# Optimization experiments

Measured on AMD Instinct MI355X. Metric: run time of the kernel, lower is better.

Reference implementation:

```python
import jax, jax.numpy as jnp
import numpy as np

N_IN = 100000   # active input voxels
N_OUT = 200000  # active output voxels after stride-2 transposed conv
K = 27          # 3x3x3 kernel offsets
INC = 64
OUTC = 64
EPS = 1e-5


def setup_inputs() -> dict:
    key = jax.random.key(0)
    ks = jax.random.split(key, 6)
    return dict(
        feats=jax.random.normal(ks[0], (N_IN, INC), jnp.float32),
        weight=jax.random.normal(ks[1], (K, INC, OUTC), jnp.float32) * 0.05,
        # kernel map: per offset, which input voxel writes to which output voxel
        in_idx=jax.random.randint(ks[2], (K, N_IN), 0, N_IN, jnp.int32),
        out_idx=jax.random.randint(ks[3], (K, N_IN), 0, N_OUT, jnp.int32),
        gamma=jnp.ones((OUTC,), jnp.float32),
        beta=jnp.zeros((OUTC,), jnp.float32),
        running_mean=jax.random.normal(ks[4], (OUTC,), jnp.float32) * 0.1,
        running_var=jax.random.uniform(ks[5], (OUTC,), jnp.float32, minval=0.5, maxval=1.5),
    )


def reference(feats, weight, in_idx, out_idx, gamma, beta, running_mean, running_var):
    """Sparse transposed conv3d (gather-matmul-scatter over kernel offsets)
    followed by eval-mode BatchNorm and ReLU, matching
    torchsparse Conv3d(transposed=True) -> BatchNorm -> ReLU(inplace)."""

    def step(out, per_offset):
        w_k, ii, oi = per_offset                 # [INC,OUTC], [M], [M]
        part = feats[ii] @ w_k                   # gather + GEMM: [M, OUTC]
        return out.at[oi].add(part), None        # scatter-add into outputs

    out0 = jnp.zeros((N_OUT, OUTC), feats.dtype)
    out, _ = jax.lax.scan(step, out0, (weight, in_idx, out_idx))

    inv_std = jax.lax.rsqrt(running_var + EPS)
    y = (out - running_mean) * (inv_std * gamma) + beta
    return jax.nn.relu(y)
```

## Files before the change

kernel.cpp:

```cpp
#include <hip/hip_runtime.h>
#include <hip/hip_bf16.h>
#include <stdint.h>

#define NIN    100000
#define NOUT   200000
#define KOFF   27
#define C      64
#define NPAIR  (KOFF * NIN)
#define EPS    1e-5f
#define NCRS   391
#define CAPC   7680
#define NBIN   128
#define IPB_F  2048
#define ACCW   65
#define FIXS   262144.0f
#define FIXI   (1.0f / 262144.0f)

typedef __attribute__((ext_vector_type(8))) short bf16x8;
typedef __attribute__((ext_vector_type(4))) float f32x4;

__global__ __launch_bounds__(256)
void cvt_bf16_kernel(const float* __restrict__ src, ushort* __restrict__ dst, int n8)
{
    int t = blockIdx.x * 256 + threadIdx.x;
    if (t >= n8) return;
    const float4* s4 = reinterpret_cast<const float4*>(src) + (size_t)t * 2;
    float4 a = s4[0], b = s4[1];
    float v[8] = {a.x, a.y, a.z, a.w, b.x, b.y, b.z, b.w};
    union { ushort u[8]; uint4 q; } pk;
    #pragma unroll
    for (int j = 0; j < 8; ++j) {
        __hip_bfloat16 h = __float2bfloat16(v[j]);
        pk.u[j] = *reinterpret_cast<ushort*>(&h);
    }
    reinterpret_cast<uint4*>(dst)[t] = pk.q;
}

__global__ __launch_bounds__(256)
void cvt_wfrag_kernel(const float* __restrict__ w, ushort* __restrict__ wfrag)
{
    int t = blockIdx.x * 256 + threadIdx.x;
    if (t >= KOFF * 4 * 2 * 64) return;
    const int lane = t & 63;
    const int f    = t >> 6;
    const int kc   = f & 1;
    const int nt   = (f >> 1) & 3;
    const int k    = f >> 3;
    const int m16  = lane & 15;
    const int q    = lane >> 4;
    union { ushort u[8]; uint4 v; } pk;
    #pragma unroll
    for (int j = 0; j < 8; ++j) {
        const int ci = kc * 32 + 8 * q + j;
        const int co = nt * 16 + m16;
        __hip_bfloat16 h = __float2bfloat16(w[(size_t)k * 4096 + ci * 64 + co]);
        pk.u[j] = *reinterpret_cast<ushort*>(&h);
    }
    reinterpret_cast<uint4*>(wfrag)[t] = pk.v;
}

__global__ __launch_bounds__(256)
void bin_coarse_kernel(const int* __restrict__ in_idx, const int* __restrict__ out_idx,
                       int* __restrict__ gcur, uint32_t* __restrict__ binned)
{
    __shared__ uint32_t staged[IPB_F];
    __shared__ ushort   sbkt[IPB_F];
    __shared__ int hist[NCRS];
    __shared__ int lbase[NCRS];
    __shared__ int gd[NCRS];
    __shared__ int cur[NCRS];
    __shared__ int s[256];

    const int t  = threadIdx.x;
    const int t0 = blockIdx.x * IPB_F;
    int n = NPAIR - t0;
    if (n < 0) n = 0;
    if (n > IPB_F) n = IPB_F;

    for (int i = t; i < NCRS; i += 256) hist[i] = 0;
    __syncthreads();

    #pragma unroll 4
    for (int j = 0; j < IPB_F / 256; ++j) {
        int i = j * 256 + t;
        if (i < n) atomicAdd(&hist[out_idx[t0 + i] >> 9], 1);
    }
    __syncthreads();

    {
        const int i0 = 2 * t, i1 = 2 * t + 1;
        int v0 = (i0 < NCRS) ? hist[i0] : 0;
        int v1 = (i1 < NCRS) ? hist[i1] : 0;
        s[t] = v0 + v1;
        __syncthreads();
        for (int off = 1; off < 256; off <<= 1) {
            int x = (t >= off) ? s[t - off] : 0;
            __syncthreads();
            s[t] += x;
            __syncthreads();
        }
        int tb = s[t] - (v0 + v1);
        if (i0 < NCRS) lbase[i0] = tb;
        if (i1 < NCRS) lbase[i1] = tb + v0;
    }
    __syncthreads();

    for (int i = t; i < NCRS; i += 256) {
        int cnt = hist[i];
        int gb  = cnt ? atomicAdd(&gcur[i], cnt) : 0;
        gd[i]   = gb - lbase[i];
        cur[i]  = lbase[i];
    }
    __syncthreads();

    #pragma unroll 4
    for (int j = 0; j < IPB_F / 256; ++j) {
        int i = j * 256 + t;
        if (i < n) {
            int tt  = t0 + i;
            int oi  = out_idx[tt];
            int k   = tt / NIN;
            int bkt = oi >> 9;
            int pos = atomicAdd(&cur[bkt], 1);
            staged[pos] = ((uint32_t)(oi & 511) << 22)
                        | ((uint32_t)k << 17)
                        | (uint32_t)in_idx[tt];
            sbkt[pos] = (ushort)bkt;
        }
    }
    __syncthreads();

    for (int i = t; i < n; i += 256) {
        int b  = sbkt[i];
        int gp = gd[b] + i;
        if ((unsigned)gp < (unsigned)CAPC)
            binned[(size_t)b * CAPC + gp] = staged[i];
    }
}

__global__ __launch_bounds__(256)
void bin_fine_kernel(const int* __restrict__ gcur, uint32_t* __restrict__ binned,
                     int* __restrict__ foff)
{
    __shared__ uint32_t staged[CAPC];
    __shared__ int hist[NBIN], base[NBIN + 1], cur[NBIN];

    const int cb = blockIdx.x;
    const int t  = threadIdx.x;
    uint32_t* seg = binned + (size_t)cb * CAPC;
    int n = gcur[cb];
    if (n > CAPC) n = CAPC;

    if (t < NBIN) hist[t] = 0;
    __syncthreads();
    for (int i = t; i < n; i += 256) {
        uint32_t pl = seg[i];
        int b = (int)(((pl >> 29) & 3) * 32 + ((pl >> 17) & 31));
        atomicAdd(&hist[b], 1);
    }
    __syncthreads();
    if (t < NBIN) base[t + 1] = hist[t];
    __syncthreads();
    for (int off = 1; off < NBIN; off <<= 1) {
        int x = 0;
        if (t < NBIN && t >= off) x = base[t + 1 - off];
        __syncthreads();
        if (t < NBIN) base[t + 1] += x;
        __syncthreads();
    }
    if (t == 0) base[0] = 0;
    __syncthreads();
    if (t < NBIN) cur[t] = base[t + 1] - hist[t];
    __syncthreads();
    for (int i = t; i < n; i += 256) {
        uint32_t pl = seg[i];
        int b = (int)(((pl >> 29) & 3) * 32 + ((pl >> 17) & 31));
        int pos = atomicAdd(&cur[b], 1);
        staged[pos] = pl;
    }
    __syncthreads();
    for (int i = t; i < n; i += 256) seg[i] = staged[i];
    if (t <= NBIN) foff[(size_t)cb * (NBIN + 1) + t] = base[t];
}

__global__ __launch_bounds__(256)
void fused_conv_kernel(const ushort* __restrict__ featsb,
                       const ushort* __restrict__ wfragb,
                       const uint32_t* __restrict__ binned,
                       const int* __restrict__ foff,
                       const float* __restrict__ gamma,
                       const float* __restrict__ beta,
                       const float* __restrict__ mean,
                       const float* __restrict__ var,
                       float* __restrict__ out)
{
    __shared__ int acc[128 * ACCW];

    const int cb   = blockIdx.x;
    const int fb   = blockIdx.y;
    const int t    = threadIdx.x;
    const int wave = t >> 6;
    const int lane = t & 63;
    const int m16  = lane & 15;
    const int q    = lane >> 4;

    for (int i = t; i < 128 * ACCW; i += 256) acc[i] = 0;
    __syncthreads();

    const uint32_t* seg = binned + (size_t)cb * CAPC;
    const int* fo = foff + (size_t)cb * (NBIN + 1) + fb * 32;
    const bf16x8* wf = reinterpret_cast<const bf16x8*>(wfragb);

    for (int k = wave; k < KOFF; k += 4) {
        const int js = fo[k], je = fo[k + 1];
        if (js >= je) continue;

        bf16x8 xf[4][2];
        #pragma unroll
        for (int nt = 0; nt < 4; ++nt)
            #pragma unroll
            for (int kc = 0; kc < 2; ++kc)
                xf[nt][kc] = wf[(size_t)((k * 4 + nt) * 2 + kc) * 64 + lane];

        for (int base = js; base < je; base += 32) {
            const int idxA    = base + m16;
            const bool validA = idxA < je;
            const uint32_t plA = seg[validA ? idxA : je - 1];
            const int iiA = plA & 0x1FFFF;
            const int lrA = (int)((plA >> 22) & 127);
            const ushort* frA = featsb + (size_t)iiA * C;
            bf16x8 yA0 = *reinterpret_cast<const bf16x8*>(frA + 8 * q);
            bf16x8 yA1 = *reinterpret_cast<const bf16x8*>(frA + 32 + 8 * q);
            if (!validA) { yA0 = bf16x8{0,0,0,0,0,0,0,0}; yA1 = bf16x8{0,0,0,0,0,0,0,0}; }

            const bool doB = (base + 16) < je;
            bf16x8 yB0, yB1;
            int lrB = 0;
            if (doB) {
                const int idxB    = base + 16 + m16;
                const bool validB = idxB < je;
                const uint32_t plB = seg[validB ? idxB : je - 1];
                const int iiB = plB & 0x1FFFF;
                lrB = (int)((plB >> 22) & 127);
                const ushort* frB = featsb + (size_t)iiB * C;
                yB0 = *reinterpret_cast<const bf16x8*>(frB + 8 * q);
                yB1 = *reinterpret_cast<const bf16x8*>(frB + 32 + 8 * q);
                if (!validB) { yB0 = bf16x8{0,0,0,0,0,0,0,0}; yB1 = bf16x8{0,0,0,0,0,0,0,0}; }
            }

            f32x4 a0 = {0,0,0,0}, a1 = {0,0,0,0}, a2 = {0,0,0,0}, a3 = {0,0,0,0};
            a0 = __builtin_amdgcn_mfma_f32_16x16x32_bf16(xf[0][0], yA0, a0, 0, 0, 0);
            a1 = __builtin_amdgcn_mfma_f32_16x16x32_bf16(xf[1][0], yA0, a1, 0, 0, 0);
            a2 = __builtin_amdgcn_mfma_f32_16x16x32_bf16(xf[2][0], yA0, a2, 0, 0, 0);
            a3 = __builtin_amdgcn_mfma_f32_16x16x32_bf16(xf[3][0], yA0, a3, 0, 0, 0);
            a0 = __builtin_amdgcn_mfma_f32_16x16x32_bf16(xf[0][1], yA1, a0, 0, 0, 0);
            a1 = __builtin_amdgcn_mfma_f32_16x16x32_bf16(xf[1][1], yA1, a1, 0, 0, 0);
            a2 = __builtin_amdgcn_mfma_f32_16x16x32_bf16(xf[2][1], yA1, a2, 0, 0, 0);
            a3 = __builtin_amdgcn_mfma_f32_16x16x32_bf16(xf[3][1], yA1, a3, 0, 0, 0);

            int* arowA = acc + lrA * ACCW + q * 4;
            #pragma unroll
            for (int r = 0; r < 4; ++r)
                atomicAdd(&arowA[ 0 + r], __float2int_rn(a0[r] * FIXS));
            #pragma unroll
            for (int r = 0; r < 4; ++r)
                atomicAdd(&arowA[16 + r], __float2int_rn(a1[r] * FIXS));
            #pragma unroll
            for (int r = 0; r < 4; ++r)
                atomicAdd(&arowA[32 + r], __float2int_rn(a2[r] * FIXS));
            #pragma unroll
            for (int r = 0; r < 4; ++r)
                atomicAdd(&arowA[48 + r], __float2int_rn(a3[r] * FIXS));

            if (doB) {
                f32x4 b0 = {0,0,0,0}, b1 = {0,0,0,0}, b2 = {0,0,0,0}, b3 = {0,0,0,0};
                b0 = __builtin_amdgcn_mfma_f32_16x16x32_bf16(xf[0][0], yB0, b0, 0, 0, 0);
                b1 = __builtin_amdgcn_mfma_f32_16x16x32_bf16(xf[1][0], yB0, b1, 0, 0, 0);
                b2 = __builtin_amdgcn_mfma_f32_16x16x32_bf16(xf[2][0], yB0, b2, 0, 0, 0);
                b3 = __builtin_amdgcn_mfma_f32_16x16x32_bf16(xf[3][0], yB0, b3, 0, 0, 0);
                b0 = __builtin_amdgcn_mfma_f32_16x16x32_bf16(xf[0][1], yB1, b0, 0, 0, 0);
                b1 = __builtin_amdgcn_mfma_f32_16x16x32_bf16(xf[1][1], yB1, b1, 0, 0, 0);
                b2 = __builtin_amdgcn_mfma_f32_16x16x32_bf16(xf[2][1], yB1, b2, 0, 0, 0);
                b3 = __builtin_amdgcn_mfma_f32_16x16x32_bf16(xf[3][1], yB1, b3, 0, 0, 0);

                int* arowB = acc + lrB * ACCW + q * 4;
                #pragma unroll
                for (int r = 0; r < 4; ++r)
                    atomicAdd(&arowB[ 0 + r], __float2int_rn(b0[r] * FIXS));
                #pragma unroll
                for (int r = 0; r < 4; ++r)
                    atomicAdd(&arowB[16 + r], __float2int_rn(b1[r] * FIXS));
                #pragma unroll
                for (int r = 0; r < 4; ++r)
                    atomicAdd(&arowB[32 + r], __float2int_rn(b2[r] * FIXS));
                #pragma unroll
                for (int r = 0; r < 4; ++r)
                    atomicAdd(&arowB[48 + r], __float2int_rn(b3[r] * FIXS));
            }
        }
    }
    __syncthreads();

    const int cp = t & 15;
    float sc[4], sh[4];
    #pragma unroll
    for (int r = 0; r < 4; ++r) {
        const int c = cp * 4 + r;
        float s = gamma[c] * rsqrtf(var[c] + EPS);
        sc[r] = s;
        sh[r] = beta[c] - mean[c] * s;
    }
    float4* out4 = reinterpret_cast<float4*>(out);
    #pragma unroll
    for (int rep = 0; rep < 8; ++rep) {
        const int i   = t + rep * 256;
        const int rl  = i >> 4;
        const int row = cb * 512 + fb * 128 + rl;
        if (row < NOUT) {
            const int* ap = &acc[rl * ACCW + cp * 4];
            float v0 = fmaf((float)ap[0] * FIXI, sc[0], sh[0]); v0 = v0 > 0.f ? v0 : 0.f;
            float v1 = fmaf((float)ap[1] * FIXI, sc[1], sh[1]); v1 = v1 > 0.f ? v1 : 0.f;
            float v2 = fmaf((float)ap[2] * FIXI, sc[2], sh[2]); v2 = v2 > 0.f ? v2 : 0.f;
            float v3 = fmaf((float)ap[3] * FIXI, sc[3], sh[3]); v3 = v3 > 0.f ? v3 : 0.f;
            out4[(size_t)row * 16 + cp] = make_float4(v0, v1, v2, v3);
        }
    }
}

__global__ __launch_bounds__(256)
void conv_scatter_kernel(const float* __restrict__ feats,
                         const float* __restrict__ weight,
                         const int*   __restrict__ in_idx,
                         const int*   __restrict__ out_idx,
                         float*       __restrict__ out)
{
    const int k    = blockIdx.y;
    const int lane = threadIdx.x & 63;
    const int wave = threadIdx.x >> 6;
    const int wavesInGrid = gridDim.x * 4;
    const int waveId      = blockIdx.x * 4 + wave;

    const float* wk = weight + (size_t)k * C * C + lane;
    float w[C];
    #pragma unroll
    for (int ci = 0; ci < C; ++ci) w[ci] = wk[(size_t)ci * C];

    const int* ii_k = in_idx  + (size_t)k * NIN;
    const int* oi_k = out_idx + (size_t)k * NIN;

    for (int r = waveId; r < NIN; r += wavesInGrid) {
        const int ii = ii_k[r];
        const int oi = oi_k[r];
        const float4* frow = reinterpret_cast<const float4*>(feats + (size_t)ii * C);
        float acc = 0.0f;
        #pragma unroll
        for (int j = 0; j < C / 4; ++j) {
            float4 f = frow[j];
            acc = fmaf(f.x, w[4 * j + 0], acc);
            acc = fmaf(f.y, w[4 * j + 1], acc);
            acc = fmaf(f.z, w[4 * j + 2], acc);
            acc = fmaf(f.w, w[4 * j + 3], acc);
        }
        atomicAdd(out + (size_t)oi * C + lane, acc);
    }
}

__global__ __launch_bounds__(256)
void bn_relu_kernel(float* __restrict__ out,
                    const float* __restrict__ gamma,
                    const float* __restrict__ beta,
                    const float* __restrict__ mean,
                    const float* __restrict__ var)
{
    const int total4 = NOUT * C / 4;
    int idx = blockIdx.x * blockDim.x + threadIdx.x;
    if (idx >= total4) return;
    const int c0 = (idx * 4) & (C - 1);
    float sc[4], sh[4];
    #pragma unroll
    for (int j = 0; j < 4; ++j) {
        const int c  = c0 + j;
        const float s = gamma[c] * rsqrtf(var[c] + EPS);
        sc[j] = s;
        sh[j] = beta[c] - mean[c] * s;
    }
    float4* p = reinterpret_cast<float4*>(out) + idx;
    float4 v = *p;
    v.x = fmaf(v.x, sc[0], sh[0]); v.x = v.x > 0.f ? v.x : 0.f;
    v.y = fmaf(v.y, sc[1], sh[1]); v.y = v.y > 0.f ? v.y : 0.f;
    v.z = fmaf(v.z, sc[2], sh[2]); v.z = v.z > 0.f ? v.z : 0.f;
    v.w = fmaf(v.w, sc[3], sh[3]); v.w = v.w > 0.f ? v.w : 0.f;
    *p = v;
}

extern "C" void kernel_launch(void* const* d_in, const int* in_sizes, int n_in,
                              void* d_out, int out_size, void* d_ws, size_t ws_size,
                              hipStream_t stream) {
    const float* feats   = (const float*)d_in[0];
    const float* weight  = (const float*)d_in[1];
    const int*   in_idx  = (const int*)  d_in[2];
    const int*   out_idx = (const int*)  d_in[3];
    const float* gamma   = (const float*)d_in[4];
    const float* beta    = (const float*)d_in[5];
    const float* rmean   = (const float*)d_in[6];
    const float* rvar    = (const float*)d_in[7];
    float* out = (float*)d_out;

    auto align = [](size_t x) { return (x + 255) & ~(size_t)255; };

    size_t a = 0;
    size_t oBin = a; a += align((size_t)NCRS * CAPC * 4);
    size_t oGc  = a; a += align((size_t)NCRS * 4);
    size_t oFo  = a; a += align((size_t)NCRS * (NBIN + 1) * 4);
    size_t oFb  = a; a += align((size_t)NIN * C * 2);
    size_t oWf  = a; a += align((size_t)KOFF * 4 * 2 * 64 * 16);

    if (ws_size < a) {
        hipMemsetAsync(out, 0, (size_t)out_size * sizeof(float), stream);
        dim3 grid(512, KOFF);
        conv_scatter_kernel<<<grid, 256, 0, stream>>>(feats, weight, in_idx, out_idx, out);
        const int total4 = NOUT * C / 4;
        bn_relu_kernel<<<(total4 + 255) / 256, 256, 0, stream>>>(out, gamma, beta, rmean, rvar);
        return;
    }

    char* ws = (char*)d_ws;
    uint32_t* binned = (uint32_t*)(ws + oBin);
    int* gcur        = (int*)(ws + oGc);
    int* foff        = (int*)(ws + oFo);
    ushort* featsb   = (ushort*)(ws + oFb);
    ushort* wfragb   = (ushort*)(ws + oWf);

    {
        int n8f = NIN * C / 8;
        cvt_bf16_kernel<<<(n8f + 255) / 256, 256, 0, stream>>>(feats, featsb, n8f);
        int nwf = KOFF * 4 * 2 * 64;
        cvt_wfrag_kernel<<<(nwf + 255) / 256, 256, 0, stream>>>(weight, wfragb);
    }

    hipMemsetAsync(gcur, 0, (size_t)NCRS * sizeof(int), stream);
    {
        int nbC = (NPAIR + IPB_F - 1) / IPB_F;
        bin_coarse_kernel<<<nbC, 256, 0, stream>>>(in_idx, out_idx, gcur, binned);
        bin_fine_kernel<<<NCRS, 256, 0, stream>>>(gcur, binned, foff);
    }

    {
        dim3 grid(NCRS, 4);
        fused_conv_kernel<<<grid, 256, 0, stream>>>(featsb, wfragb, binned, foff,
                                                    gamma, beta, rmean, rvar, out);
    }
}
```

Baseline: 187.9 us.

## Split output channels across a third grid dimension and fold fixed-point scale into inputs

Adds blockIdx.z to split the 64 output channels into two halves, so each block keeps a half-width LDS accumulator (33 ints per row) and holds only the weight fragments for its half. This doubles the block count and halves the LDS footprint per block to raise occupancy and reduce atomic contention per block. The fixed-point scale is moved into the bf16 conversion by multiplying both feats and weights by 512, which removes the per-element multiply before the integer atomics. The cost is that every feature-row gather is repeated in both channel halves, and the BN scale and shift are now recomputed per output element.

Measured after the change: 201.9 us. +7.5%, slower.

```diff
diff --git a/kernel.cpp b/kernel.cpp
--- a/kernel.cpp
+++ b/kernel.cpp
@@ -12,8 +12,7 @@
 #define CAPC   7680
 #define NBIN   128
 #define IPB_F  2048
-#define ACCW   65
-#define FIXS   262144.0f
+#define ACW    33
 #define FIXI   (1.0f / 262144.0f)
 
 typedef __attribute__((ext_vector_type(8))) short bf16x8;
@@ -30,7 +29,7 @@
     union { ushort u[8]; uint4 q; } pk;
     #pragma unroll
     for (int j = 0; j < 8; ++j) {
-        __hip_bfloat16 h = __float2bfloat16(v[j]);
+        __hip_bfloat16 h = __float2bfloat16(v[j] * 512.0f);
         pk.u[j] = *reinterpret_cast<ushort*>(&h);
     }
     reinterpret_cast<uint4*>(dst)[t] = pk.q;
@@ -53,7 +52,7 @@
     for (int j = 0; j < 8; ++j) {
         const int ci = kc * 32 + 8 * q + j;
         const int co = nt * 16 + m16;
-        __hip_bfloat16 h = __float2bfloat16(w[(size_t)k * 4096 + ci * 64 + co]);
+        __hip_bfloat16 h = __float2bfloat16(w[(size_t)k * 4096 + ci * 64 + co] * 512.0f);
         pk.u[j] = *reinterpret_cast<ushort*>(&h);
     }
     reinterpret_cast<uint4*>(wfrag)[t] = pk.v;
@@ -194,17 +193,18 @@
                        const float* __restrict__ var,
                        float* __restrict__ out)
 {
-    __shared__ int acc[128 * ACCW];
+    __shared__ int acc[128 * ACW];
 
     const int cb   = blockIdx.x;
     const int fb   = blockIdx.y;
+    const int zc   = blockIdx.z;
     const int t    = threadIdx.x;
     const int wave = t >> 6;
     const int lane = t & 63;
     const int m16  = lane & 15;
     const int q    = lane >> 4;
 
-    for (int i = t; i < 128 * ACCW; i += 256) acc[i] = 0;
+    for (int i = t; i < 128 * ACW; i += 256) acc[i] = 0;
     __syncthreads();
 
     const uint32_t* seg = binned + (size_t)cb * CAPC;
@@ -215,12 +215,12 @@
         const int js = fo[k], je = fo[k + 1];
         if (js >= je) continue;
 
-        bf16x8 xf[4][2];
+        bf16x8 xf[2][2];
         #pragma unroll
-        for (int nt = 0; nt < 4; ++nt)
+        for (int ntl = 0; ntl < 2; ++ntl)
             #pragma unroll
             for (int kc = 0; kc < 2; ++kc)
-                xf[nt][kc] = wf[(size_t)((k * 4 + nt) * 2 + kc) * 64 + lane];
+                xf[ntl][kc] = wf[(size_t)((k * 4 + zc * 2 + ntl) * 2 + kc) * 64 + lane];
 
         for (int base = js; base < je; base += 32) {
             const int idxA    = base + m16;
@@ -234,7 +234,7 @@
             if (!validA) { yA0 = bf16x8{0,0,0,0,0,0,0,0}; yA1 = bf16x8{0,0,0,0,0,0,0,0}; }
 
             const bool doB = (base + 16) < je;
-            bf16x8 yB0, yB1;
+            bf16x8 yB0 = {0,0,0,0,0,0,0,0}, yB1 = {0,0,0,0,0,0,0,0};
             int lrB = 0;
             if (doB) {
                 const int idxB    = base + 16 + m16;
@@ -248,81 +248,60 @@
                 if (!validB) { yB0 = bf16x8{0,0,0,0,0,0,0,0}; yB1 = bf16x8{0,0,0,0,0,0,0,0}; }
             }
 
-            f32x4 a0 = {0,0,0,0}, a1 = {0,0,0,0}, a2 = {0,0,0,0}, a3 = {0,0,0,0};
-            a0 = __builtin_amdgcn_mfma_f32_16x16x32_bf16(xf[0][0], yA0, a0, 0, 0, 0);
-            a1 = __builtin_amdgcn_mfma_f32_16x16x32_bf16(xf[1][0], yA0, a1, 0, 0, 0);
-            a2 = __builtin_amdgcn_mfma_f32_16x16x32_bf16(xf[2][0], yA0, a2, 0, 0, 0);
-            a3 = __builtin_amdgcn_mfma_f32_16x16x32_bf16(xf[3][0], yA0, a3, 0, 0, 0);
-            a0 = __builtin_amdgcn_mfma_f32_16x16x32_bf16(xf[0][1], yA1, a0, 0, 0, 0);
-            a1 = __builtin_amdgcn_mfma_f32_16x16x32_bf16(xf[1][1], yA1, a1, 0, 0, 0);
-            a2 = __builtin_amdgcn_mfma_f32_16x16x32_bf16(xf[2][1], yA1, a2, 0, 0, 0);
-            a3 = __builtin_amdgcn_mfma_f32_16x16x32_bf16(xf[3][1], yA1, a3, 0, 0, 0);
-
-            int* arowA = acc + lrA * ACCW + q * 4;
-            #pragma unroll
-            for (int r = 0; r < 4; ++r)
-                atomicAdd(&arowA[ 0 + r], __float2int_rn(a0[r] * FIXS));
-            #pragma unroll
-            for (int r = 0; r < 4; ++r)
-                atomicAdd(&arowA[16 + r], __float2int_rn(a1[r] * FIXS));
-            #pragma unroll
-            for (int r = 0; r < 4; ++r)
-                atomicAdd(&arowA[32 + r], __float2int_rn(a2[r] * FIXS));
-            #pragma unroll
-            for (int r = 0; r < 4; ++r)
-                atomicAdd(&arowA[48 + r], __float2int_rn(a3[r] * FIXS));
-
-            if (doB) {
-                f32x4 b0 = {0,0,0,0}, b1 = {0,0,0,0}, b2 = {0,0,0,0}, b3 = {0,0,0,0};
-                b0 = __builtin_amdgcn_mfma_f32_16x16x32_bf16(xf[0][0], yB0, b0, 0, 0, 0);
-                b1 = __builtin_amdgcn_mfma_f32_16x16x32_bf16(xf[1][0], yB0, b1, 0, 0, 0);
-                b2 = __builtin_amdgcn_mfma_f32_16x16x32_bf16(xf[2][0], yB0, b2, 0, 0, 0);
-                b3 = __builtin_amdgcn_mfma_f32_16x16x32_bf16(xf[3][0], yB0, b3, 0, 0, 0);
-                b0 = __builtin_amdgcn_mfma_f32_16x16x32_bf16(xf[0][1], yB1, b0, 0, 0, 0);
-                b1 = __builtin_amdgcn_mfma_f32_16x16x32_bf16(xf[1][1], yB1, b1, 0, 0, 0);
-                b2 = __builtin_amdgcn_mfma_f32_16x16x32_bf16(xf[2][1], yB1, b2, 0, 0, 0);
-                b3 = __builtin_amdgcn_mfma_f32_16x16x32_bf16(xf[3][1], yB1, b3, 0, 0, 0);
-
-                int* arowB = acc + lrB * ACCW + q * 4;
+            {
+                f32x4 c0 = {0,0,0,0}, c1 = {0,0,0,0};
+                c0 = __builtin_amdgcn_mfma_f32_16x16x32_bf16(xf[0][0], yA0, c0, 0, 0, 0);
+                c1 = __builtin_amdgcn_mfma_f32_16x16x32_bf16(xf[1][0], yA0, c1, 0, 0, 0);
+                c0 = __builtin_amdgcn_mfma_f32_16x16x32_bf16(xf[0][1], yA1, c0, 0, 0, 0);
+                c1 = __builtin_amdgcn_mfma_f32_16x16x32_bf16(xf[1][1], yA1, c1, 0, 0, 0);
+                int* arow = acc + lrA * ACW + q * 4;
                 #pragma unroll
                 for (int r = 0; r < 4; ++r)
-                    atomicAdd(&arowB[ 0 + r], __float2int_rn(b0[r] * FIXS));
+                    atomicAdd(&arow[ 0 + r], __float2int_rn(c0[r]));
                 #pragma unroll
                 for (int r = 0; r < 4; ++r)
-                    atomicAdd(&arowB[16 + r], __float2int_rn(b1[r] * FIXS));
+                    atomicAdd(&arow[16 + r], __float2int_rn(c1[r]));
+            }
+
+            if (doB) {
+                f32x4 c0 = {0,0,0,0}, c1 = {0,0,0,0};
+                c0 = __builtin_amdgcn_mfma_f32_16x16x32_bf16(xf[0][0], yB0, c0, 0, 0, 0);
+                c1 = __builtin_amdgcn_mfma_f32_16x16x32_bf16(xf[1][0], yB0, c1, 0, 0, 0);
+                c0 = __builtin_amdgcn_mfma_f32_16x16x32_bf16(xf[0][1], yB1, c0, 0, 0, 0);
+                c1 = __builtin_amdgcn_mfma_f32_16x16x32_bf16(xf[1][1], yB1, c1, 0, 0, 0);
+                int* arow = acc + lrB * ACW + q * 4;
                 #pragma unroll
                 for (int r = 0; r < 4; ++r)
-                    atomicAdd(&arowB[32 + r], __float2int_rn(b2[r] * FIXS));
+                    atomicAdd(&arow[ 0 + r], __float2int_rn(c0[r]));
                 #pragma unroll
                 for (int r = 0; r < 4; ++r)
-                    atomicAdd(&arowB[48 + r], __float2int_rn(b3[r] * FIXS));
+                    atomicAdd(&arow[16 + r], __float2int_rn(c1[r]));
             }
         }
     }
     __syncthreads();
 
-    const int cp = t & 15;
-    float sc[4], sh[4];
-    #pragma unroll
-    for (int r = 0; r < 4; ++r) {
-        const int c = cp * 4 + r;
-        float s = gamma[c] * rsqrtf(var[c] + EPS);
-        sc[r] = s;
-        sh[r] = beta[c] - mean[c] * s;
-    }
     float4* out4 = reinterpret_cast<float4*>(out);
     #pragma unroll
-    for (int rep = 0; rep < 8; ++rep) {
+    for (int rep = 0; rep < 4; ++rep) {
         const int i   = t + rep * 256;
-        const int rl  = i >> 4;
+        const int rl  = i >> 3;
+        const int cp8 = i & 7;
         const int row = cb * 512 + fb * 128 + rl;
         if (row < NOUT) {
-            const int* ap = &acc[rl * ACCW + cp * 4];
-            float v0 = fmaf((float)ap[0] * FIXI, sc[0], sh[0]); v0 = v0 > 0.f ? v0 : 0.f;
-            float v1 = fmaf((float)ap[1] * FIXI, sc[1], sh[1]); v1 = v1 > 0.f ? v1 : 0.f;
-            float v2 = fmaf((float)ap[2] * FIXI, sc[2], sh[2]); v2 = v2 > 0.f ? v2 : 0.f;
-            float v3 = fmaf((float)ap[3] * FIXI, sc[3], sh[3]); v3 = v3 > 0.f ? v3 : 0.f;
-            out4[(size_t)row * 16 + cp] = make_float4(v0, v1, v2, v3);
+            const int c0 = zc * 32 + cp8 * 4;
+            const int* ap = &acc[rl * ACW + cp8 * 4];
+            float4 v;
+            float* vp = reinterpret_cast<float*>(&v);
+            #pragma unroll
+            for (int r = 0; r < 4; ++r) {
+                const int c = c0 + r;
+                float s  = gamma[c] * rsqrtf(var[c] + EPS);
+                float sh = beta[c] - mean[c] * s;
+                float y  = fmaf((float)ap[r] * FIXI, s, sh);
+                vp[r] = y > 0.f ? y : 0.f;
+            }
+            out4[(size_t)row * 16 + zc * 8 + cp8] = v;
         }
     }
 }
@@ -446,7 +425,7 @@
     }
 
     {
-        dim3 grid(NCRS, 4);
+        dim3 grid(NCRS, 4, 2);
         fused_conv_kernel<<<grid, 256, 0, stream>>>(featsb, wfragb, binned, foff,
                                                     gamma, beta, rmean, rvar, out);
     }
```
